# Optimization experiments

Hardware: AMD Instinct MI355X
Metric: run time of the kernel (lower is better)

Reference implementation:

```python
import jax, jax.numpy as jnp
import numpy as np

N = 16384      # number of nodes
U = 128        # feature units
AVG_DEGREE = 32


def setup_inputs() -> dict:
    key = jax.random.key(0)
    kx, ka, kw = jax.random.split(key, 3)
    x = jax.random.normal(kx, (N, U), dtype=jnp.float32)
    # Sparse binary adjacency (avg degree ~32), stored dense because the
    # original module densifies it via tf.sparse.to_dense before matmul.
    adj = (jax.random.uniform(ka, (N, N)) < (AVG_DEGREE / N)).astype(jnp.float32)
    W = jax.random.normal(kw, (U, U), dtype=jnp.float32) * 0.05  # 'random_normal' init
    b = jnp.zeros((U,), dtype=jnp.float32)
    return {"x": x, "adj": adj, "W": W, "b": b}


def reference(x, adj, W, b):
    adj = jax.lax.stop_gradient(adj)
    # hop 1: aggregate neighbors, dense linear, swish
    neigh1 = adj @ x                      # [N, U]
    x1 = jax.nn.swish(neigh1 @ W + b)     # [N, U]
    # hop 2: same weights W, b (shared across both hops in the original)
    neigh2 = adj @ x1                     # [N, U]
    x2 = jax.nn.swish(neigh2 @ W + b)     # [N, U]
    return x2
```

## Files before the change

kernel.cpp:

```cpp
#include <hip/hip_runtime.h>
#include <hip/hip_bf16.h>
#include <stdint.h>

#define NN 16384
#define UU 128
#define CAP 128
#define LCAP 8

typedef unsigned short u16;
typedef unsigned int uv4 __attribute__((ext_vector_type(4)));

__device__ __forceinline__ float4 gather_row_sum_f32(const float* __restrict__ src,
                                                     const u16* sIdx, int c,
                                                     int half, int sl) {
    float4 acc = {0.f, 0.f, 0.f, 0.f};
#pragma unroll 8
    for (int k = half; k < c; k += 2) {
        const int j = sIdx[k];
        const float4 v = *reinterpret_cast<const float4*>(src + (size_t)j * UU + sl * 4);
        acc.x += v.x; acc.y += v.y; acc.z += v.z; acc.w += v.w;
    }
    acc.x += __shfl_xor(acc.x, 32);
    acc.y += __shfl_xor(acc.y, 32);
    acc.z += __shfl_xor(acc.z, 32);
    acc.w += __shfl_xor(acc.w, 32);
    return acc;
}

template <typename OutT>
__device__ __forceinline__ void block_linear_swish(const float (*sNeigh)[UU],
                                                   const float* __restrict__ W,
                                                   const float* __restrict__ bias,
                                                   OutT* __restrict__ dst,
                                                   int rowBase, int tid) {
    const int u = tid & 127;
    const int g = tid >> 7;
    const float bu = bias[u];
    float f0 = bu, f1 = bu;
    for (int v = 0; v < UU; ++v) {
        const float w = W[v * UU + u];
        f0 += sNeigh[2 * g + 0][v] * w;
        f1 += sNeigh[2 * g + 1][v] * w;
    }
    const float s0 = f0 / (1.0f + __expf(-f0));
    const float s1 = f1 / (1.0f + __expf(-f1));
    const size_t i0 = (size_t)(rowBase + 2 * g + 0) * UU + u;
    const size_t i1 = (size_t)(rowBase + 2 * g + 1) * UU + u;
    if constexpr (sizeof(OutT) == 2) {
        dst[i0] = __float2bfloat16(s0);
        dst[i1] = __float2bfloat16(s1);
    } else {
        dst[i0] = s0;
        dst[i1] = s1;
    }
}

__global__ __launch_bounds__(256) void fused_sparsify_hop1(
    const float* __restrict__ adj, const float* __restrict__ x,
    const float* __restrict__ W, const float* __restrict__ bias,
    __hip_bfloat16* __restrict__ x1, u16* __restrict__ ell,
    unsigned* __restrict__ cnt) {
    __shared__ u16   raw[4][64 * LCAP];
    __shared__ u16   sIdx[4][CAP];
    __shared__ float sNeigh[4][UU];

    const int tid  = threadIdx.x;
    const int wave = tid >> 6;
    const int lane = tid & 63;
    const int rowBase = blockIdx.x * 4;
    const int row  = rowBase + wave;

    const uv4* rowp = reinterpret_cast<const uv4*>(adj + (size_t)row * NN);
    u16* myraw = &raw[wave][lane * LCAP];
    int myCnt = 0;

    uv4 c0 = __builtin_nontemporal_load(&rowp[0 * 64 + lane]);
    uv4 c1 = __builtin_nontemporal_load(&rowp[1 * 64 + lane]);
    uv4 c2 = __builtin_nontemporal_load(&rowp[2 * 64 + lane]);
    uv4 c3 = __builtin_nontemporal_load(&rowp[3 * 64 + lane]);

    for (int b = 0; b < 16; ++b) {
        uv4 n0 = c0, n1 = c1, n2 = c2, n3 = c3;
        if (b < 15) {
            const uv4* nb = rowp + (size_t)(b + 1) * 256 + lane;
            n0 = __builtin_nontemporal_load(nb + 0 * 64);
            n1 = __builtin_nontemporal_load(nb + 1 * 64);
            n2 = __builtin_nontemporal_load(nb + 2 * 64);
            n3 = __builtin_nontemporal_load(nb + 3 * 64);
        }
        const uv4 vv[4] = {c0, c1, c2, c3};
#pragma unroll
        for (int j = 0; j < 4; ++j) {
            const unsigned colBase = (unsigned)(((b * 4 + j) * 64 + lane) * 4);
            const unsigned vals[4] = {vv[j].x, vv[j].y, vv[j].z, vv[j].w};
#pragma unroll
            for (int e = 0; e < 4; ++e) {
                if (vals[e] != 0u) {
                    if (myCnt < LCAP) myraw[myCnt] = (u16)(colBase + e);
                    ++myCnt;
                }
            }
        }
        c0 = n0; c1 = n1; c2 = n2; c3 = n3;
    }
    if (myCnt > LCAP) myCnt = LCAP;

    int pre = myCnt;
#pragma unroll
    for (int d = 1; d < 64; d <<= 1) {
        int t = __shfl_up(pre, d);
        if (lane >= d) pre += t;
    }
    const int excl  = pre - myCnt;
    const int total = __shfl(pre, 63);
    const int c = (total < CAP) ? total : CAP;
    if (lane == 0) cnt[row] = (unsigned)c;

    for (int i = 0; i < myCnt; ++i) {
        const int pos = excl + i;
        if (pos < CAP) sIdx[wave][pos] = myraw[i];
    }

    for (int p = lane; p < c; p += 64) ell[(size_t)row * CAP + p] = sIdx[wave][p];

    const int half = lane >> 5;
    const int sl   = lane & 31;
    float4 acc = gather_row_sum_f32(x, sIdx[wave], c, half, sl);
    if (half == 0) *reinterpret_cast<float4*>(&sNeigh[wave][sl * 4]) = acc;
    __syncthreads();

    block_linear_swish(sNeigh, W, bias, x1, rowBase, tid);
}

__global__ __launch_bounds__(256) void fused_hop2(
    const __hip_bfloat16* __restrict__ x1, const u16* __restrict__ ell,
    const unsigned* __restrict__ cnt, const float* __restrict__ W,
    const float* __restrict__ bias, float* __restrict__ out) {
    __shared__ u16   sIdx[4][CAP];
    __shared__ float sNeigh[4][UU];

    const int tid  = threadIdx.x;
    const int wave = tid >> 6;
    const int lane = tid & 63;
    const int rowBase = blockIdx.x * 4;
    const int row  = rowBase + wave;

    const int c = (int)cnt[row];
    const ushort2* ellRow = reinterpret_cast<const ushort2*>(ell + (size_t)row * CAP);
    reinterpret_cast<ushort2*>(sIdx[wave])[lane] = ellRow[lane];

    const int q = lane >> 4;
    const int s = lane & 15;
    float a[8] = {0.f, 0.f, 0.f, 0.f, 0.f, 0.f, 0.f, 0.f};
#pragma unroll 4
    for (int k = q; k < c; k += 4) {
        const int j = sIdx[wave][k];
        const uv4 v = *reinterpret_cast<const uv4*>(
            reinterpret_cast<const u16*>(x1) + (size_t)j * UU + s * 8);
        const unsigned d[4] = {v.x, v.y, v.z, v.w};
#pragma unroll
        for (int m = 0; m < 4; ++m) {
            a[2 * m]     += __uint_as_float(d[m] << 16);
            a[2 * m + 1] += __uint_as_float(d[m] & 0xffff0000u);
        }
    }
#pragma unroll
    for (int m = 0; m < 8; ++m) {
        a[m] += __shfl_xor(a[m], 16);
        a[m] += __shfl_xor(a[m], 32);
    }
    if (q == 0) {
        float4 lo = {a[0], a[1], a[2], a[3]};
        float4 hi = {a[4], a[5], a[6], a[7]};
        *reinterpret_cast<float4*>(&sNeigh[wave][s * 8])     = lo;
        *reinterpret_cast<float4*>(&sNeigh[wave][s * 8 + 4]) = hi;
    }
    __syncthreads();

    block_linear_swish(sNeigh, W, bias, out, rowBase, tid);
}

extern "C" void kernel_launch(void* const* d_in, const int* in_sizes, int n_in,
                              void* d_out, int out_size, void* d_ws, size_t ws_size,
                              hipStream_t stream) {
    const float* x   = (const float*)d_in[0];
    const float* adj = (const float*)d_in[1];
    const float* W   = (const float*)d_in[2];
    const float* b   = (const float*)d_in[3];
    float* out = (float*)d_out;

    char* ws = (char*)d_ws;
    __hip_bfloat16* x1  = (__hip_bfloat16*)(ws);
    u16*            ell = (u16*)(ws + (size_t)4 * 1024 * 1024);
    unsigned*       cnt = (unsigned*)(ws + (size_t)8 * 1024 * 1024);

    fused_sparsify_hop1<<<NN / 4, 256, 0, stream>>>(adj, x, W, b, x1, ell, cnt);
    fused_hop2<<<NN / 4, 256, 0, stream>>>(x1, ell, cnt, W, b, out);
}
```

Measured before the change: 221.9 us.

## Reassociate hop2 as adj@(x1@W) with separate dense GEMM kernel

Hop 2 is reordered so that x1@W is computed first in a new dense GEMM kernel (bf16 W and x1 staged in shared memory, 32 rows per block). The gather kernel then sums the pre-transformed y1 rows and applies bias and swish directly, with no per-row matvec in the gather kernel. This removes the 4-rows-per-block 128x128 matvec work from the gather path but adds an extra launch and another round trip of the intermediate through global memory. Rounding y1 and W to bf16 before aggregation changes the precision profile.

```diff
diff --git a/kernel.cpp b/kernel.cpp
--- a/kernel.cpp
+++ b/kernel.cpp
@@ -27,12 +27,11 @@
     return acc;
 }
 
-template <typename OutT>
-__device__ __forceinline__ void block_linear_swish(const float (*sNeigh)[UU],
-                                                   const float* __restrict__ W,
-                                                   const float* __restrict__ bias,
-                                                   OutT* __restrict__ dst,
-                                                   int rowBase, int tid) {
+__device__ __forceinline__ void block_linear_swish_bf16(const float (*sNeigh)[UU],
+                                                        const float* __restrict__ W,
+                                                        const float* __restrict__ bias,
+                                                        u16* __restrict__ dst,
+                                                        int rowBase, int tid) {
     const int u = tid & 127;
     const int g = tid >> 7;
     const float bu = bias[u];
@@ -44,22 +43,14 @@
     }
     const float s0 = f0 / (1.0f + __expf(-f0));
     const float s1 = f1 / (1.0f + __expf(-f1));
-    const size_t i0 = (size_t)(rowBase + 2 * g + 0) * UU + u;
-    const size_t i1 = (size_t)(rowBase + 2 * g + 1) * UU + u;
-    if constexpr (sizeof(OutT) == 2) {
-        dst[i0] = __float2bfloat16(s0);
-        dst[i1] = __float2bfloat16(s1);
-    } else {
-        dst[i0] = s0;
-        dst[i1] = s1;
-    }
+    dst[(size_t)(rowBase + 2 * g + 0) * UU + u] = __bfloat16_as_ushort(__float2bfloat16(s0));
+    dst[(size_t)(rowBase + 2 * g + 1) * UU + u] = __bfloat16_as_ushort(__float2bfloat16(s1));
 }
 
 __global__ __launch_bounds__(256) void fused_sparsify_hop1(
     const float* __restrict__ adj, const float* __restrict__ x,
     const float* __restrict__ W, const float* __restrict__ bias,
-    __hip_bfloat16* __restrict__ x1, u16* __restrict__ ell,
-    unsigned* __restrict__ cnt) {
+    u16* __restrict__ x1, u16* __restrict__ ell, unsigned* __restrict__ cnt) {
     __shared__ u16   raw[4][64 * LCAP];
     __shared__ u16   sIdx[4][CAP];
     __shared__ float sNeigh[4][UU];
@@ -129,21 +120,72 @@
     if (half == 0) *reinterpret_cast<float4*>(&sNeigh[wave][sl * 4]) = acc;
     __syncthreads();
 
-    block_linear_swish(sNeigh, W, bias, x1, rowBase, tid);
-}
-
-__global__ __launch_bounds__(256) void fused_hop2(
-    const __hip_bfloat16* __restrict__ x1, const u16* __restrict__ ell,
-    const unsigned* __restrict__ cnt, const float* __restrict__ W,
-    const float* __restrict__ bias, float* __restrict__ out) {
-    __shared__ u16   sIdx[4][CAP];
-    __shared__ float sNeigh[4][UU];
+    block_linear_swish_bf16(sNeigh, W, bias, x1, rowBase, tid);
+}
+
+__global__ __launch_bounds__(256) void gemm_y1(const u16* __restrict__ x1,
+                                               const float* __restrict__ W,
+                                               u16* __restrict__ y1) {
+    __shared__ u16   sW[UU * UU];
+    __shared__ float sX[32][UU];
+
+    const int tid = threadIdx.x;
+    const int rowBase = blockIdx.x * 32;
+
+    {
+        const float2* Wf2 = reinterpret_cast<const float2*>(W);
+        unsigned* sW32 = reinterpret_cast<unsigned*>(sW);
+        for (int i = tid; i < UU * UU / 2; i += 256) {
+            const float2 w2 = Wf2[i];
+            sW32[i] = ((unsigned)__bfloat16_as_ushort(__float2bfloat16(w2.x))) |
+                      (((unsigned)__bfloat16_as_ushort(__float2bfloat16(w2.y))) << 16);
+        }
+    }
+    {
+        const uv4* src = reinterpret_cast<const uv4*>(x1 + (size_t)rowBase * UU);
+        float* dstBase = &sX[0][0];
+        for (int i = tid; i < 32 * UU / 8; i += 256) {
+            const uv4 v = src[i];
+            float* dst = dstBase + i * 8;
+            const unsigned d[4] = {v.x, v.y, v.z, v.w};
+#pragma unroll
+            for (int m = 0; m < 4; ++m) {
+                dst[2 * m]     = __uint_as_float(d[m] << 16);
+                dst[2 * m + 1] = __uint_as_float(d[m] & 0xffff0000u);
+            }
+        }
+    }
+    __syncthreads();
+
+    const int u = tid & 127;
+    const int g = tid >> 7;
+    float acc[16];
+#pragma unroll
+    for (int r = 0; r < 16; ++r) acc[r] = 0.f;
+
+    for (int v = 0; v < UU; ++v) {
+        const float w = __uint_as_float((unsigned)sW[v * UU + u] << 16);
+#pragma unroll
+        for (int r = 0; r < 16; ++r)
+            acc[r] += sX[g * 16 + r][v] * w;
+    }
+#pragma unroll
+    for (int r = 0; r < 16; ++r)
+        y1[(size_t)(rowBase + g * 16 + r) * UU + u] =
+            __bfloat16_as_ushort(__float2bfloat16(acc[r]));
+}
+
+__global__ __launch_bounds__(256) void hop2_lite(const u16* __restrict__ y1,
+                                                 const u16* __restrict__ ell,
+                                                 const unsigned* __restrict__ cnt,
+                                                 const float* __restrict__ bias,
+                                                 float* __restrict__ out) {
+    __shared__ u16 sIdx[4][CAP];
 
     const int tid  = threadIdx.x;
     const int wave = tid >> 6;
     const int lane = tid & 63;
-    const int rowBase = blockIdx.x * 4;
-    const int row  = rowBase + wave;
+    const int row  = blockIdx.x * 4 + wave;
 
     const int c = (int)cnt[row];
     const ushort2* ellRow = reinterpret_cast<const ushort2*>(ell + (size_t)row * CAP);
@@ -152,11 +194,10 @@
     const int q = lane >> 4;
     const int s = lane & 15;
     float a[8] = {0.f, 0.f, 0.f, 0.f, 0.f, 0.f, 0.f, 0.f};
-#pragma unroll 4
+#pragma unroll 8
     for (int k = q; k < c; k += 4) {
         const int j = sIdx[wave][k];
-        const uv4 v = *reinterpret_cast<const uv4*>(
-            reinterpret_cast<const u16*>(x1) + (size_t)j * UU + s * 8);
+        const uv4 v = *reinterpret_cast<const uv4*>(y1 + (size_t)j * UU + s * 8);
         const unsigned d[4] = {v.x, v.y, v.z, v.w};
 #pragma unroll
         for (int m = 0; m < 4; ++m) {
@@ -170,14 +211,20 @@
         a[m] += __shfl_xor(a[m], 32);
     }
     if (q == 0) {
-        float4 lo = {a[0], a[1], a[2], a[3]};
-        float4 hi = {a[4], a[5], a[6], a[7]};
-        *reinterpret_cast<float4*>(&sNeigh[wave][s * 8])     = lo;
-        *reinterpret_cast<float4*>(&sNeigh[wave][s * 8 + 4]) = hi;
-    }
-    __syncthreads();
-
-    block_linear_swish(sNeigh, W, bias, out, rowBase, tid);
+        const float4 b0 = reinterpret_cast<const float4*>(bias)[s * 2];
+        const float4 b1 = reinterpret_cast<const float4*>(bias)[s * 2 + 1];
+        const float bb[8] = {b0.x, b0.y, b0.z, b0.w, b1.x, b1.y, b1.z, b1.w};
+        float o[8];
+#pragma unroll
+        for (int m = 0; m < 8; ++m) {
+            const float p = a[m] + bb[m];
+            o[m] = p / (1.0f + __expf(-p));
+        }
+        float4 o0 = {o[0], o[1], o[2], o[3]};
+        float4 o1 = {o[4], o[5], o[6], o[7]};
+        *reinterpret_cast<float4*>(out + (size_t)row * UU + s * 8)     = o0;
+        *reinterpret_cast<float4*>(out + (size_t)row * UU + s * 8 + 4) = o1;
+    }
 }
 
 extern "C" void kernel_launch(void* const* d_in, const int* in_sizes, int n_in,
@@ -190,10 +237,12 @@
     float* out = (float*)d_out;
 
     char* ws = (char*)d_ws;
-    __hip_bfloat16* x1  = (__hip_bfloat16*)(ws);
-    u16*            ell = (u16*)(ws + (size_t)4 * 1024 * 1024);
-    unsigned*       cnt = (unsigned*)(ws + (size_t)8 * 1024 * 1024);
+    u16*      x1  = (u16*)(ws);
+    u16*      y1  = (u16*)(ws + (size_t)4 * 1024 * 1024);
+    u16*      ell = (u16*)(ws + (size_t)8 * 1024 * 1024);
+    unsigned* cnt = (unsigned*)(ws + (size_t)12 * 1024 * 1024);
 
     fused_sparsify_hop1<<<NN / 4, 256, 0, stream>>>(adj, x, W, b, x1, ell, cnt);
-    fused_hop2<<<NN / 4, 256, 0, stream>>>(x1, ell, cnt, W, b, out);
-}
+    gemm_y1<<<NN / 32, 256, 0, stream>>>(x1, W, y1);
+    hop2_lite<<<NN / 4, 256, 0, stream>>>(y1, ell, cnt, b, out);
+}
```

New measurement: 228.3 us. 2.9% more time.
